# Kernel optimization log

Hardware: AMD Instinct MI355X
Metric: run time of the kernel (lower is better)

## Reference

```python
import jax, jax.numpy as jnp
import numpy as np

WS = 8          # window_size
NH = 8          # num_heads
IQKV = 128      # inner_qk_v_dim
IQKC = 32       # inner_qk_c_dim
IVV = 64        # inner_v_v_dim
EPS = 1e-6
B, HH, WW, DV, DC = 2, 224, 224, 256, 64


def _rmsnorm(x, g):
    return x * jax.lax.rsqrt(jnp.mean(x * x, axis=-1, keepdims=True) + EPS) * g


def _window(x):
    # (b, h, w, d) -> (b, Wh, Ww, ws*ws, d)
    b, h, w, d = x.shape
    x = x.reshape(b, h // WS, WS, w // WS, WS, d).transpose(0, 1, 3, 2, 4, 5)
    return x.reshape(b, h // WS, w // WS, WS * WS, d)


def _unwindow(x, h, w):
    # (b, N, ws*ws, d) -> (b, h, w, d)
    b, _, _, d = x.shape
    x = x.reshape(b, h // WS, w // WS, WS, WS, d).transpose(0, 1, 3, 2, 4, 5)
    return x.reshape(b, h, w, d)


def _source_qkv(V, C, Wqk_v, bqk_v, g_v, Wqk_c, bqk_c, g_c, Wv):
    Vw, Cw = _window(V), _window(C)          # (b, Wh, Ww, n, d)
    b, Wh, Ww, n, _ = Vw.shape
    N = Wh * Ww
    Vavg, Cavg = Vw.mean(-2), Cw.mean(-2)
    qk_v = _rmsnorm(Vavg @ Wqk_v + bqk_v, g_v)   # (b, Wh, Ww, 2*IQKV)
    qk_c = _rmsnorm(Cavg @ Wqk_c + bqk_c, g_c)   # (b, Wh, Ww, 2*IQKC)
    # 'b Wh Ww (H e) -> b H (Wh Ww) e' then chunk2 along e
    qk_v = qk_v.reshape(b, N, NH, -1).transpose(0, 2, 1, 3)
    qk_c = qk_c.reshape(b, N, NH, -1).transpose(0, 2, 1, 3)
    ev, ec = qk_v.shape[-1] // 2, qk_c.shape[-1] // 2
    qv, kv = qk_v[..., :ev], qk_v[..., ev:]
    qc, kc = qk_c[..., :ec], qk_c[..., ec:]
    # value projection: 'b Wh Ww n (e H) -> b H (Wh Ww) (n e)'
    e = IVV // NH
    Vv = (Vw @ Wv).reshape(b, N, n, e, NH).transpose(0, 4, 1, 2, 3).reshape(b, NH, N, n * e)
    return qv, kv, qc, kc, Vv, (Wh, Ww)


def _forward(values0, coords0, values1, coords1,
             Wqk_v, bqk_v, g_v, Wqk_c, bqk_c, g_c, Wv, Wback):
    parts = [_source_qkv(V, C, Wqk_v, bqk_v, g_v, Wqk_c, bqk_c, g_c, Wv)
             for V, C in ((values0, coords0), (values1, coords1))]
    qv = jnp.concatenate([p[0] for p in parts], axis=2)
    kv = jnp.concatenate([p[1] for p in parts], axis=2)
    qc = jnp.concatenate([p[2] for p in parts], axis=2)
    kc = jnp.concatenate([p[3] for p in parts], axis=2)
    Vv = jnp.concatenate([p[4] for p in parts], axis=2)
    scores = (jnp.einsum('bhqe,bhke->bhqk', qv, kv) / jnp.sqrt(jnp.float32(IQKV))
              + jnp.einsum('bhqe,bhke->bhqk', qc, kc) / jnp.sqrt(jnp.float32(IQKC)))
    A = jax.nn.softmax(scores, axis=-1)            # (b, H, N, N)
    rw = jnp.einsum('bhqk,bhkf->bhqf', A, Vv)      # (b, H, N, n*e)
    b, _, N, _ = rw.shape
    n, e = WS * WS, IVV // NH
    # 'b H N (n e) -> b N n (e H)'
    rw = rw.reshape(b, NH, N, n, e).transpose(0, 2, 3, 4, 1).reshape(b, N, n, e * NH)
    rw = rw @ Wback                                # (b, N, n, Dv)
    outs, off = [], 0
    for (V, _), p in zip(((values0, coords0), (values1, coords1)), parts):
        Wh, Ww = p[5]
        Ns = Wh * Ww
        outs.append(_unwindow(rw[:, off:off + Ns], Wh * WS, Ww * WS))
        off += Ns
    return tuple(outs)


def setup_inputs() -> dict:
    key = jax.random.key(0)
    ks = jax.random.split(key, 8)
    s = 0.02
    return {
        'values0': jax.random.normal(ks[0], (B, HH, WW, DV), jnp.float32),
        'coords0': jax.random.normal(ks[1], (B, HH, WW, DC), jnp.float32),
        'values1': jax.random.normal(ks[2], (B, HH, WW, DV), jnp.float32),
        'coords1': jax.random.normal(ks[3], (B, HH, WW, DC), jnp.float32),
        'Wqk_v': s * jax.random.normal(ks[4], (DV, 2 * IQKV), jnp.float32),
        'bqk_v': jnp.zeros((2 * IQKV,), jnp.float32),
        'g_v': jnp.ones((2 * IQKV,), jnp.float32),
        'Wqk_c': s * jax.random.normal(ks[5], (DC, 2 * IQKC), jnp.float32),
        'bqk_c': jnp.zeros((2 * IQKC,), jnp.float32),
        'g_c': jnp.ones((2 * IQKC,), jnp.float32),
        'Wv': s * jax.random.normal(ks[6], (DV, IVV), jnp.float32),
        'Wback': s * jax.random.normal(ks[7], (IVV, DV), jnp.float32),
    }


def reference(values0, coords0, values1, coords1,
              Wqk_v, bqk_v, g_v, Wqk_c, bqk_c, g_c, Wv, Wback):
    return _forward(values0, coords0, values1, coords1,
                    Wqk_v, bqk_v, g_v, Wqk_c, bqk_c, g_c, Wv, Wback)
```

## Files before the change

kernel.cpp:

```cpp
#include <hip/hip_runtime.h>

#define NSRC 784
#define NTOT 1568
#define NHD 8
#define DVC 256
#define DCC 64
#define D20 20
#define FDIM 512
#define OUT_PER_SRC 25690112

typedef short s16x8 __attribute__((ext_vector_type(8)));
typedef unsigned short u16x8 __attribute__((ext_vector_type(8)));
typedef unsigned short u16x4 __attribute__((ext_vector_type(4)));
typedef float f32x4 __attribute__((ext_vector_type(4)));
typedef float f32x16 __attribute__((ext_vector_type(16)));
typedef unsigned u32x4 __attribute__((ext_vector_type(4)));

__device__ __forceinline__ unsigned short f2bf(float x) {
    unsigned u = __float_as_uint(x);
    unsigned r = (u + 0x7FFFu + ((u >> 16) & 1u)) >> 16;
    return (unsigned short)r;
}

__device__ __forceinline__ unsigned cvt_pk_bf16(float lo, float hi) {
    unsigned r;
    asm volatile("v_cvt_pk_bf16_f32 %0, %1, %2" : "=v"(r) : "v"(lo), "v"(hi));
    return r;
}

__device__ __forceinline__ void split_bf(float x, unsigned short& hi, unsigned short& lo) {
    unsigned short h = f2bf(x);
    float hf = __uint_as_float(((unsigned)h) << 16);
    hi = h;
    lo = f2bf(x - hf);
}

__global__ __launch_bounds__(256) void kz_zero(unsigned short* __restrict__ p) {
    size_t i = (size_t)blockIdx.x * 256 + threadIdx.x;
    u16x8 z = (u16x8)0;
    *(u16x8*)&p[i * 8] = z;
}

__global__ __launch_bounds__(256) void k0_wsplit(
    const float* __restrict__ Wv,
    unsigned short* __restrict__ WThi, unsigned short* __restrict__ WTlo) {
    int e = blockIdx.x, dd = threadIdx.x;
    float x = Wv[dd * DCC + e];
    unsigned short h, l;
    split_bf(x, h, l);
    WThi[e * 256 + dd] = h;
    WTlo[e * 256 + dd] = l;
}

__global__ __launch_bounds__(256) void k0b_wback(
    const float* __restrict__ Wb, unsigned short* __restrict__ Wp) {
    int idx = blockIdx.x * 256 + threadIdx.x;
    int jj = idx & 7, lane = (idx >> 3) & 63, hl = (idx >> 9) & 1;
    int kc = (idx >> 10) & 1, mt = idx >> 11;
    int c = mt * 16 + (lane & 15);
    int j = kc * 32 + (lane >> 4) * 8 + jj;
    unsigned short h, l;
    split_bf(Wb[j * 256 + c], h, l);
    Wp[idx] = hl ? l : h;
}

__global__ __launch_bounds__(256) void k1c_avg(
    const float* __restrict__ c0, const float* __restrict__ c1,
    float* __restrict__ Cavg) {
    int wi = blockIdx.x * 4 + (threadIdx.x >> 6);
    int d = threadIdx.x & 63;
    int b = wi / NTOT, N = wi % NTOT;
    int src = N / NSRC, nloc = N % NSRC;
    int wh = nloc / 28, ww = nloc % 28;
    const float* __restrict__ C = src ? c1 : c0;
    int pbase = (b * 224 + wh * 8) * 224 + ww * 8;
    float s = 0.f;
#pragma unroll 8
    for (int p = 0; p < 64; ++p)
        s += C[(size_t)(pbase + (p >> 3) * 224 + (p & 7)) * DCC + d];
    Cavg[(size_t)wi * DCC + d] = s * 0.015625f;
}

__global__ __launch_bounds__(256) void k2_qk(
    const float* __restrict__ Vavg, const float* __restrict__ Cavg,
    const float* __restrict__ Wqkv, const float* __restrict__ bqkv, const float* __restrict__ gv,
    const float* __restrict__ Wqkc, const float* __restrict__ bqkc, const float* __restrict__ gc,
    unsigned short* __restrict__ Qp, unsigned short* __restrict__ Kp) {
    __shared__ float xv[DVC];
    __shared__ float xc[DCC];
    __shared__ float wred[4];
    int blk = blockIdx.x;
    int b = blk / NTOT, N = blk % NTOT;
    int t = threadIdx.x;
    int tile = N >> 5, l31 = N & 31;
    xv[t] = Vavg[(size_t)blk * DVC + t];
    if (t < DCC) xc[t] = Cavg[(size_t)blk * DCC + t];
    __syncthreads();
    float yv = bqkv[t];
#pragma unroll 4
    for (int d = 0; d < DVC; ++d) yv += xv[d] * Wqkv[d * 256 + t];
    float ss = yv * yv;
#pragma unroll
    for (int off = 32; off; off >>= 1) ss += __shfl_xor(ss, off, 64);
    if ((t & 63) == 0) wred[t >> 6] = ss;
    __syncthreads();
    float tot = wred[0] + wred[1] + wred[2] + wred[3];
    float rv = rsqrtf(tot * (1.f / 256.f) + 1e-6f);
    float yn = yv * rv * gv[t];
    int h = t >> 5, c = t & 31;
    int bh = b * NHD + h;
    {
        int isq = (c < 16);
        int d = isq ? c : c - 16;
        float val = isq ? yn * 0.088388347648318447f : yn;
        unsigned short h16, l16;
        split_bf(val, h16, l16);
        int hh = d >> 3, j = d & 7;
        size_t base = ((size_t)(bh * 49 + tile) * 4) * 512 + (size_t)(hh * 32 + l31) * 8 + j;
        unsigned short* dst = isq ? Qp : Kp;
        dst[base] = h16;
        dst[base + 1024] = l16;
    }
    if (t < DCC) {
        float yc = bqkc[t];
#pragma unroll 4
        for (int d = 0; d < DCC; ++d) yc += xc[d] * Wqkc[d * 64 + t];
        float sc = yc * yc;
#pragma unroll
        for (int off = 32; off; off >>= 1) sc += __shfl_xor(sc, off, 64);
        float rc = rsqrtf(sc * (1.f / 64.f) + 1e-6f);
        float ycn = yc * rc * gc[t];
        int h2 = t >> 3, c2 = t & 7;
        int bh2 = b * NHD + h2;
        int isq = (c2 < 4);
        int dd = isq ? c2 : c2 - 4;
        float val = isq ? ycn * 0.17677669529663687f : ycn;
        unsigned short h16, l16;
        split_bf(val, h16, l16);
        size_t base = ((size_t)(bh2 * 49 + tile) * 4 + 1) * 512 + (size_t)l31 * 8 + dd;
        unsigned short* dst = isq ? Qp : Kp;
        dst[base] = h16;
        dst[base + 1024] = l16;
    }
}

__global__ __launch_bounds__(256) void k3_vv(
    const float* __restrict__ v0, const float* __restrict__ v1,
    const unsigned short* __restrict__ WThi, const unsigned short* __restrict__ WTlo,
    unsigned short* __restrict__ Vvb, float* __restrict__ Vavg) {
    __shared__ unsigned short Ahi[64 * 128];
    __shared__ unsigned short Alo[64 * 128];
    int blk = blockIdx.x;
    int b = blk / NTOT, N = blk % NTOT;
    int src = N / NSRC, nloc = N % NSRC;
    int wh = nloc / 28, ww = nloc % 28;
    const float* __restrict__ V = src ? v1 : v0;
    int t = threadIdx.x;
    int w = t >> 6, lane = t & 63;
    int lm = lane & 15, lk = lane >> 4;
    int pxw = w * 16;
    int lhalf = lane >> 5;
    int d4 = (lane & 31) * 4;
    int pbase = (b * 224 + wh * 8) * 224 + ww * 8;

    float ap[8] = {0.f, 0.f, 0.f, 0.f, 0.f, 0.f, 0.f, 0.f};
    f32x4 acc4[4];
#pragma unroll
    for (int nt = 0; nt < 4; ++nt) acc4[nt] = (f32x4)0.f;

#pragma unroll
    for (int ph = 0; ph < 2; ++ph) {
        int d0 = ph * 128;
        float4 xs[8];
#pragma unroll
        for (int i = 0; i < 8; ++i) {
            int px = pxw + i * 2 + lhalf;
            xs[i] = *(const float4*)&V[(size_t)(pbase + (px >> 3) * 224 + (px & 7)) * DVC + d0 + d4];
        }
#pragma unroll
        for (int i = 0; i < 8; ++i) {
            ap[ph * 4 + 0] += xs[i].x; ap[ph * 4 + 1] += xs[i].y;
            ap[ph * 4 + 2] += xs[i].z; ap[ph * 4 + 3] += xs[i].w;
        }
        if (ph) __syncthreads();
#pragma unroll
        for (int i = 0; i < 8; ++i) {
            int px = pxw + i * 2 + lhalf;
            u16x4 h4, l4;
            unsigned short hq, lq;
            split_bf(xs[i].x, hq, lq); h4[0] = hq; l4[0] = lq;
            split_bf(xs[i].y, hq, lq); h4[1] = hq; l4[1] = lq;
            split_bf(xs[i].z, hq, lq); h4[2] = hq; l4[2] = lq;
            split_bf(xs[i].w, hq, lq); h4[3] = hq; l4[3] = lq;
            int addr = px * 128 + (((d4 >> 3) ^ (px & 7)) << 3) + (d4 & 7);
            *(u16x4*)&Ahi[addr] = h4;
            *(u16x4*)&Alo[addr] = l4;
        }
        __syncthreads();
#pragma unroll
        for (int c2 = 0; c2 < 4; ++c2) {
            int dd0 = c2 * 32;
            s16x8 Bh4[4], Bl4[4];
#pragma unroll
            for (int nt = 0; nt < 4; ++nt) {
                int e = nt * 16 + lm;
                Bh4[nt] = *(const s16x8*)&WThi[e * 256 + d0 + dd0 + lk * 8];
                Bl4[nt] = *(const s16x8*)&WTlo[e * 256 + d0 + dd0 + lk * 8];
            }
            int row = pxw + lm;
            int raddr = row * 128 + ((((dd0 >> 3) + lk) ^ (row & 7)) << 3);
            s16x8 ahi = *(const s16x8*)&Ahi[raddr];
            s16x8 alo = *(const s16x8*)&Alo[raddr];
#pragma unroll
            for (int nt = 0; nt < 4; ++nt) {
                acc4[nt] = __builtin_amdgcn_mfma_f32_16x16x32_bf16(ahi, Bl4[nt], acc4[nt], 0, 0, 0);
                acc4[nt] = __builtin_amdgcn_mfma_f32_16x16x32_bf16(alo, Bh4[nt], acc4[nt], 0, 0, 0);
                acc4[nt] = __builtin_amdgcn_mfma_f32_16x16x32_bf16(ahi, Bh4[nt], acc4[nt], 0, 0, 0);
            }
        }
    }
    __syncthreads();
    unsigned short* eb = Ahi;
#pragma unroll
    for (int nt = 0; nt < 4; ++nt) {
        int e = nt * 16 + lm;
#pragma unroll
        for (int r = 0; r < 4; ++r) {
            int px = pxw + lk * 4 + r;
            eb[px * 66 + e] = f2bf(acc4[nt][r]);
        }
    }
#pragma unroll
    for (int j = 0; j < 8; ++j) ap[j] += __shfl_xor(ap[j], 32, 64);
    float* avgb = (float*)Alo;
    if (lhalf == 0) {
#pragma unroll
        for (int ph = 0; ph < 2; ++ph) {
            float4 v4 = make_float4(ap[ph * 4], ap[ph * 4 + 1], ap[ph * 4 + 2], ap[ph * 4 + 3]);
            *(float4*)&avgb[w * 256 + ph * 128 + d4] = v4;
        }
    }
    __syncthreads();
    unsigned short* dst = Vvb + (size_t)blk * 4096;
#pragma unroll
    for (int i = 0; i < 2; ++i) {
        int flat16 = i * 256 + t;
        int f3 = flat16 >> 6;
        int h = (flat16 >> 3) & 7;
        int px8 = (flat16 & 7) * 8;
        u16x8 vv;
#pragma unroll
        for (int u = 0; u < 8; ++u) vv[u] = eb[(px8 + u) * 66 + f3 * 8 + h];
        *(u16x8*)&dst[flat16 * 8] = vv;
    }
    Vavg[(size_t)blk * DVC + t] =
        (avgb[t] + avgb[256 + t] + avgb[512 + t] + avgb[768 + t]) * 0.015625f;
}

__global__ __launch_bounds__(256) void k3b_pack(
    const unsigned short* __restrict__ Vvb, unsigned short* __restrict__ Vp) {
    __shared__ unsigned short tile[32 * 576];
    int kt = blockIdx.x, bh = blockIdx.y;
    int b = bh >> 3, h = bh & 7;
    int t = threadIdx.x;
#pragma unroll
    for (int it = 0; it < 8; ++it) {
        int flat = it * 256 + t;
        int r5 = flat >> 6;
        int c = flat & 63;
        int f3 = c >> 3, px8 = (c & 7) * 8;
        const unsigned short* s =
            Vvb + ((size_t)(b * NTOT + kt * 32 + r5) * 8 + f3) * 512 + h * 64 + px8;
        *(u16x8*)&tile[r5 * 576 + f3 * 72 + px8] = *(const u16x8*)s;
    }
    __syncthreads();
    unsigned short* dst = Vp + ((size_t)bh * 49 + kt) * 16384;
#pragma unroll
    for (int it = 0; it < 8; ++it) {
        int flato = it * 256 + t;
        int lane = flato & 63;
        int kh = (flato >> 6) & 1;
        int sub = (flato >> 7) & 3;
        int w = flato >> 9;
        int l31 = lane & 31, hh = lane >> 5;
        int f = w * 128 + sub * 32 + l31;
        int kbase = kh * 16 + hh * 8;
        u16x8 v;
#pragma unroll
        for (int j = 0; j < 8; ++j)
            v[j] = tile[(kbase + j) * 576 + (f & 7) * 72 + (f >> 3)];
        *(u16x8*)&dst[(size_t)flato * 8] = v;
    }
}

__global__ __launch_bounds__(256) void k4_attn(
    const unsigned short* __restrict__ Qp, const unsigned short* __restrict__ Kp,
    const unsigned short* __restrict__ Vp, float* __restrict__ rw) {
    __shared__ float ebuf[32 * 132];
    int wg = blockIdx.x;
    int qt = wg >> 4, bh = wg & 15;
    int q0 = qt * 32;
    int t = threadIdx.x;
    int w = t >> 6, lane = t & 63;
    int l31 = lane & 31, hh = lane >> 5;

    const unsigned short* __restrict__ Qpb = Qp + ((size_t)(bh * 49 + qt) * 4) * 512 + lane * 8;
    const unsigned short* __restrict__ Kpb = Kp + (size_t)bh * 49 * 2048 + lane * 8;
    const unsigned short* __restrict__ Vpb = Vp + (size_t)bh * 49 * 16384 + lane * 8;

    s16x8 qa0 = *(const s16x8*)&Qpb[0];
    s16x8 qa1 = *(const s16x8*)&Qpb[512];
    s16x8 ql0 = *(const s16x8*)&Qpb[1024];
    s16x8 ql1 = *(const s16x8*)&Qpb[1536];

    s16x8 ka0 = *(const s16x8*)&Kpb[0];
    s16x8 ka1 = *(const s16x8*)&Kpb[512];
    s16x8 kl0 = *(const s16x8*)&Kpb[1024];
    s16x8 kl1 = *(const s16x8*)&Kpb[1536];

    float m = -1e30f, lsum = 0.f;
    f32x16 acc[4];
#pragma unroll
    for (int s = 0; s < 4; ++s) acc[s] = (f32x16)0.f;

    for (int kt = 0; kt < NTOT / 32; ++kt) {
        const unsigned short* Vtile = Vpb + (size_t)kt * 16384 + (w * 8) * 512;
        s16x8 va[8];
#pragma unroll
        for (int fr = 0; fr < 8; ++fr)
            va[fr] = *(const s16x8*)&Vtile[fr * 512];
        int ktn = (kt < 48) ? kt + 1 : 48;
        const unsigned short* Ktn = Kpb + (size_t)ktn * 2048;
        s16x8 kn0 = *(const s16x8*)&Ktn[0];
        s16x8 kn1 = *(const s16x8*)&Ktn[512];
        s16x8 kn2 = *(const s16x8*)&Ktn[1024];
        s16x8 kn3 = *(const s16x8*)&Ktn[1536];

        f32x16 sacc = (f32x16)0.f;
        sacc = __builtin_amdgcn_mfma_f32_32x32x16_bf16(kl0, qa0, sacc, 0, 0, 0);
        sacc = __builtin_amdgcn_mfma_f32_32x32x16_bf16(ka0, ql0, sacc, 0, 0, 0);
        sacc = __builtin_amdgcn_mfma_f32_32x32x16_bf16(ka0, qa0, sacc, 0, 0, 0);
        sacc = __builtin_amdgcn_mfma_f32_32x32x16_bf16(kl1, qa1, sacc, 0, 0, 0);
        sacc = __builtin_amdgcn_mfma_f32_32x32x16_bf16(ka1, ql1, sacc, 0, 0, 0);
        sacc = __builtin_amdgcn_mfma_f32_32x32x16_bf16(ka1, qa1, sacc, 0, 0, 0);

        float tmax = sacc[0];
#pragma unroll
        for (int r = 1; r < 16; ++r) tmax = fmaxf(tmax, sacc[r]);
        tmax = fmaxf(tmax, __shfl_xor(tmax, 32, 64));
        if (__any(tmax > m + 8.f)) {
            float mn = fmaxf(m, tmax);
            float sc = __expf(m - mn);
#pragma unroll
            for (int s = 0; s < 4; ++s) acc[s] = acc[s] * sc;
            lsum *= sc;
            m = mn;
        }
        unsigned P2[8];
        float tsum = 0.f;
#pragma unroll
        for (int j = 0; j < 8; ++j) {
            float pa = __expf(sacc[2 * j] - m);
            float pb = __expf(sacc[2 * j + 1] - m);
            tsum += pa + pb;
            P2[j] = cvt_pk_bf16(pa, pb);
        }
        lsum += tsum + __shfl_xor(tsum, 32, 64);
        unsigned X2[8];
#pragma unroll
        for (int j = 0; j < 8; ++j) X2[j] = (unsigned)__shfl_xor((int)P2[j], 32, 64);
        u32x4 b0u, b1u;
        if (hh == 0) {
            b0u[0] = P2[0]; b0u[1] = P2[1]; b0u[2] = X2[0]; b0u[3] = X2[1];
            b1u[0] = P2[4]; b1u[1] = P2[5]; b1u[2] = X2[4]; b1u[3] = X2[5];
        } else {
            b0u[0] = X2[2]; b0u[1] = X2[3]; b0u[2] = P2[2]; b0u[3] = P2[3];
            b1u[0] = X2[6]; b1u[1] = X2[7]; b1u[2] = P2[6]; b1u[3] = P2[7];
        }
        s16x8 pb0 = __builtin_bit_cast(s16x8, b0u);
        s16x8 pb1 = __builtin_bit_cast(s16x8, b1u);

#pragma unroll
        for (int sub = 0; sub < 4; ++sub) {
            acc[sub] = __builtin_amdgcn_mfma_f32_32x32x16_bf16(va[2 * sub],     pb0, acc[sub], 0, 0, 0);
            acc[sub] = __builtin_amdgcn_mfma_f32_32x32x16_bf16(va[2 * sub + 1], pb1, acc[sub], 0, 0, 0);
        }
        ka0 = kn0; ka1 = kn1; kl0 = kn2; kl1 = kn3;
    }

    float inv = 1.f / lsum;
    float* rwg = rw + ((size_t)bh * NTOT + q0) * FDIM;
#pragma unroll
    for (int c = 0; c < 4; ++c) {
        __syncthreads();
        if (w == c) {
#pragma unroll
            for (int sub = 0; sub < 4; ++sub) {
#pragma unroll
                for (int r = 0; r < 16; ++r) {
                    int fl = sub * 32 + (r & 3) + 8 * (r >> 2) + 4 * hh;
                    ebuf[l31 * 132 + fl] = acc[sub][r] * inv;
                }
            }
        }
        __syncthreads();
        int qr = t >> 3, cb = (t & 7) * 16;
#pragma unroll
        for (int j = 0; j < 4; ++j) {
            *(float4*)&rwg[(size_t)qr * FDIM + c * 128 + cb + j * 4] =
                *(const float4*)&ebuf[qr * 132 + cb + j * 4];
        }
    }
}

__global__ __launch_bounds__(256) void k5_back(
    const float* __restrict__ rw, const unsigned short* __restrict__ Wp,
    float* __restrict__ out) {
    __shared__ unsigned short SB[2 * 64 * 72];
    unsigned short* BhL = SB;
    unsigned short* BlL = SB + 64 * 72;
    int blk = blockIdx.x;
    int b = blk / NTOT, N = blk % NTOT;
    int src = N / NSRC, nloc = N % NSRC;
    int wh = nloc / 28, ww = nloc % 28;
    int t = threadIdx.x;
    int w = t >> 6, lane = t & 63;
    int lm = lane & 15, lk = lane >> 4;
    int pbase = (b * 224 + wh * 8) * 224 + ww * 8;

#pragma unroll
    for (int i = 0; i < 4; ++i) {
        int flat4 = i * 256 + t;
        int h = flat4 >> 7;
        int f0 = (flat4 & 127) * 4;
        float4 v = *(const float4*)&rw[((size_t)(b * NHD + h) * NTOT + N) * FDIM + f0];
        int n = f0 >> 3;
        int ebase = f0 & 7;
        float vv[4] = {v.x, v.y, v.z, v.w};
#pragma unroll
        for (int u = 0; u < 4; ++u) {
            int j8 = ebase + u;
            unsigned short h16, l16;
            split_bf(vv[u], h16, l16);
            int col = ((j8 ^ (n & 7)) << 3) | h;
            BhL[n * 72 + col] = h16;
            BlL[n * 72 + col] = l16;
        }
    }
    __syncthreads();

    f32x4 acc[4][4];
#pragma unroll
    for (int mi = 0; mi < 4; ++mi)
#pragma unroll
        for (int nt = 0; nt < 4; ++nt) acc[mi][nt] = (f32x4)0.f;

    const unsigned short* Wpw = Wp + (size_t)(w * 4) * 2048 + lane * 8;
#pragma unroll
    for (int kc = 0; kc < 2; ++kc) {
        s16x8 Ah[4], Al[4], Bh4[4], Bl4[4];
#pragma unroll
        for (int mi = 0; mi < 4; ++mi) {
            int base = mi * 2048 + kc * 1024;
            Ah[mi] = *(const s16x8*)&Wpw[base];
            Al[mi] = *(const s16x8*)&Wpw[base + 512];
        }
#pragma unroll
        for (int nt = 0; nt < 4; ++nt) {
            int n = nt * 16 + lm;
            int addr = n * 72 + (((kc * 4 + lk) ^ (n & 7)) << 3);
            Bh4[nt] = *(const s16x8*)&BhL[addr];
            Bl4[nt] = *(const s16x8*)&BlL[addr];
        }
#pragma unroll
        for (int mi = 0; mi < 4; ++mi)
#pragma unroll
            for (int nt = 0; nt < 4; ++nt) {
                acc[mi][nt] = __builtin_amdgcn_mfma_f32_16x16x32_bf16(Ah[mi], Bl4[nt], acc[mi][nt], 0, 0, 0);
                acc[mi][nt] = __builtin_amdgcn_mfma_f32_16x16x32_bf16(Al[mi], Bh4[nt], acc[mi][nt], 0, 0, 0);
                acc[mi][nt] = __builtin_amdgcn_mfma_f32_16x16x32_bf16(Ah[mi], Bh4[nt], acc[mi][nt], 0, 0, 0);
            }
    }

    float* eb = (float*)SB;
    float* outp = out + (size_t)src * OUT_PER_SRC;
#pragma unroll
    for (int ch = 0; ch < 4; ++ch) {
        __syncthreads();
        if (w == ch) {
#pragma unroll
            for (int mi = 0; mi < 4; ++mi)
#pragma unroll
                for (int nt = 0; nt < 4; ++nt)
#pragma unroll
                    for (int r = 0; r < 4; ++r) {
                        int n = nt * 16 + lm;
                        int cl = mi * 16 + lk * 4 + r;
                        eb[n * 68 + cl] = acc[mi][nt][r];
                    }
        }
        __syncthreads();
#pragma unroll
        for (int i = 0; i < 4; ++i) {
            int fl4 = i * 256 + t;
            int n = fl4 >> 4, c4 = (fl4 & 15) * 4;
            int opix = pbase + (n >> 3) * 224 + (n & 7);
            *(float4*)&outp[(size_t)opix * DVC + ch * 64 + c4] =
                *(const float4*)&eb[n * 68 + c4];
        }
    }
}

extern "C" void kernel_launch(void* const* d_in, const int* in_sizes, int n_in,
                              void* d_out, int out_size, void* d_ws, size_t ws_size,
                              hipStream_t stream) {
    const float* v0   = (const float*)d_in[0];
    const float* c0   = (const float*)d_in[1];
    const float* v1   = (const float*)d_in[2];
    const float* c1   = (const float*)d_in[3];
    const float* Wqkv = (const float*)d_in[4];
    const float* bqkv = (const float*)d_in[5];
    const float* gv   = (const float*)d_in[6];
    const float* Wqkc = (const float*)d_in[7];
    const float* bqkc = (const float*)d_in[8];
    const float* gc   = (const float*)d_in[9];
    const float* Wv   = (const float*)d_in[10];
    const float* Wbk  = (const float*)d_in[11];

    float* ws = (float*)d_ws;
    float* rw   = ws;
    float* Vavg = ws;
    float* Cavg = ws + 802816;
    unsigned short* Qp   = (unsigned short*)(ws + 12845056);
    unsigned short* Kp   = (unsigned short*)(ws + 13647872);
    unsigned short* WThi = (unsigned short*)(ws + 14450688);
    unsigned short* WTlo = (unsigned short*)(ws + 14458880);
    unsigned short* Vvb  = (unsigned short*)(ws + 14467072);
    unsigned short* Vp   = (unsigned short*)(ws + 20889600);
    unsigned short* Wp   = (unsigned short*)(ws + 27312128);

    float* outp = (float*)d_out;

    kz_zero  <<<1568, 256, 0, stream>>>(Qp);
    k0_wsplit<<<64, 256, 0, stream>>>(Wv, WThi, WTlo);
    k0b_wback<<<256, 256, 0, stream>>>(Wbk, Wp);
    k3_vv    <<<2 * NTOT, 256, 0, stream>>>(v0, v1, WThi, WTlo, Vvb, Vavg);
    k1c_avg  <<<784, 256, 0, stream>>>(c0, c1, Cavg);
    k2_qk    <<<2 * NTOT, 256, 0, stream>>>(Vavg, Cavg, Wqkv, bqkv, gv, Wqkc, bqkc, gc, Qp, Kp);
    k3b_pack <<<dim3(49, 16), 256, 0, stream>>>(Vvb, Vp);
    k4_attn  <<<784, 256, 0, stream>>>(Qp, Kp, Vp, rw);
    k5_back  <<<2 * NTOT, 256, 0, stream>>>(rw, Wp, outp);
}
```

Baseline: 359.0 us.

## Feed window pixels directly as MFMA operands and prepack Wv in fragment layout

The value-projection kernel no longer stages split bf16 input tiles through shared memory. Each lane now loads its own pixel's eight channels straight from global memory and uses them as the B operand, with Wv prepacked hi/lo into MFMA fragment order so each weight fragment is one contiguous vector load. The per-window channel averages are computed with cross-lane shuffles instead of per-thread accumulation, which removes two barriers and the large LDS buffers. The cost is more shuffle work for the averages and strided 32-byte global loads per lane.

```diff
diff --git a/kernel.cpp b/kernel.cpp
--- a/kernel.cpp
+++ b/kernel.cpp
@@ -41,15 +41,16 @@
     *(u16x8*)&p[i * 8] = z;
 }
 
-__global__ __launch_bounds__(256) void k0_wsplit(
-    const float* __restrict__ Wv,
-    unsigned short* __restrict__ WThi, unsigned short* __restrict__ WTlo) {
-    int e = blockIdx.x, dd = threadIdx.x;
-    float x = Wv[dd * DCC + e];
+__global__ __launch_bounds__(256) void k0c_wvpack(
+    const float* __restrict__ Wv, unsigned short* __restrict__ Wvp) {
+    int idx = blockIdx.x * 256 + threadIdx.x;
+    int j = idx & 7, lane = (idx >> 3) & 63, hl = (idx >> 9) & 1;
+    int c = (idx >> 10) & 7, mi = idx >> 13;
+    int e = mi * 16 + (lane & 15);
+    int dd = c * 32 + (lane >> 4) * 8 + j;
     unsigned short h, l;
-    split_bf(x, h, l);
-    WThi[e * 256 + dd] = h;
-    WTlo[e * 256 + dd] = l;
+    split_bf(Wv[dd * DCC + e], h, l);
+    Wvp[idx] = hl ? l : h;
 }
 
 __global__ __launch_bounds__(256) void k0b_wback(
@@ -146,10 +147,10 @@
 
 __global__ __launch_bounds__(256) void k3_vv(
     const float* __restrict__ v0, const float* __restrict__ v1,
-    const unsigned short* __restrict__ WThi, const unsigned short* __restrict__ WTlo,
+    const unsigned short* __restrict__ Wvp,
     unsigned short* __restrict__ Vvb, float* __restrict__ Vavg) {
-    __shared__ unsigned short Ahi[64 * 128];
-    __shared__ unsigned short Alo[64 * 128];
+    __shared__ unsigned short eb[64 * 66];
+    __shared__ float avgw[1024];
     int blk = blockIdx.x;
     int b = blk / NTOT, N = blk % NTOT;
     int src = N / NSRC, nloc = N % NSRC;
@@ -158,86 +159,55 @@
     int t = threadIdx.x;
     int w = t >> 6, lane = t & 63;
     int lm = lane & 15, lk = lane >> 4;
-    int pxw = w * 16;
-    int lhalf = lane >> 5;
-    int d4 = (lane & 31) * 4;
+    int px = w * 16 + lm;
     int pbase = (b * 224 + wh * 8) * 224 + ww * 8;
-
-    float ap[8] = {0.f, 0.f, 0.f, 0.f, 0.f, 0.f, 0.f, 0.f};
-    f32x4 acc4[4];
-#pragma unroll
-    for (int nt = 0; nt < 4; ++nt) acc4[nt] = (f32x4)0.f;
-
-#pragma unroll
-    for (int ph = 0; ph < 2; ++ph) {
-        int d0 = ph * 128;
-        float4 xs[8];
-#pragma unroll
-        for (int i = 0; i < 8; ++i) {
-            int px = pxw + i * 2 + lhalf;
-            xs[i] = *(const float4*)&V[(size_t)(pbase + (px >> 3) * 224 + (px & 7)) * DVC + d0 + d4];
-        }
-#pragma unroll
-        for (int i = 0; i < 8; ++i) {
-            ap[ph * 4 + 0] += xs[i].x; ap[ph * 4 + 1] += xs[i].y;
-            ap[ph * 4 + 2] += xs[i].z; ap[ph * 4 + 3] += xs[i].w;
-        }
-        if (ph) __syncthreads();
-#pragma unroll
-        for (int i = 0; i < 8; ++i) {
-            int px = pxw + i * 2 + lhalf;
-            u16x4 h4, l4;
+    const float* __restrict__ xrow =
+        V + (size_t)(pbase + (px >> 3) * 224 + (px & 7)) * DVC + lk * 8;
+
+    f32x4 acc[4];
+#pragma unroll
+    for (int mi = 0; mi < 4; ++mi) acc[mi] = (f32x4)0.f;
+
+#pragma unroll
+    for (int c = 0; c < 8; ++c) {
+        float4 x0 = *(const float4*)&xrow[c * 32];
+        float4 x1 = *(const float4*)&xrow[c * 32 + 4];
+        float xv8[8] = {x0.x, x0.y, x0.z, x0.w, x1.x, x1.y, x1.z, x1.w};
+        u16x8 bhu, blu;
+#pragma unroll
+        for (int j = 0; j < 8; ++j) {
             unsigned short hq, lq;
-            split_bf(xs[i].x, hq, lq); h4[0] = hq; l4[0] = lq;
-            split_bf(xs[i].y, hq, lq); h4[1] = hq; l4[1] = lq;
-            split_bf(xs[i].z, hq, lq); h4[2] = hq; l4[2] = lq;
-            split_bf(xs[i].w, hq, lq); h4[3] = hq; l4[3] = lq;
-            int addr = px * 128 + (((d4 >> 3) ^ (px & 7)) << 3) + (d4 & 7);
-            *(u16x4*)&Ahi[addr] = h4;
-            *(u16x4*)&Alo[addr] = l4;
-        }
-        __syncthreads();
-#pragma unroll
-        for (int c2 = 0; c2 < 4; ++c2) {
-            int dd0 = c2 * 32;
-            s16x8 Bh4[4], Bl4[4];
-#pragma unroll
-            for (int nt = 0; nt < 4; ++nt) {
-                int e = nt * 16 + lm;
-                Bh4[nt] = *(const s16x8*)&WThi[e * 256 + d0 + dd0 + lk * 8];
-                Bl4[nt] = *(const s16x8*)&WTlo[e * 256 + d0 + dd0 + lk * 8];
-            }
-            int row = pxw + lm;
-            int raddr = row * 128 + ((((dd0 >> 3) + lk) ^ (row & 7)) << 3);
-            s16x8 ahi = *(const s16x8*)&Ahi[raddr];
-            s16x8 alo = *(const s16x8*)&Alo[raddr];
-#pragma unroll
-            for (int nt = 0; nt < 4; ++nt) {
-                acc4[nt] = __builtin_amdgcn_mfma_f32_16x16x32_bf16(ahi, Bl4[nt], acc4[nt], 0, 0, 0);
-                acc4[nt] = __builtin_amdgcn_mfma_f32_16x16x32_bf16(alo, Bh4[nt], acc4[nt], 0, 0, 0);
-                acc4[nt] = __builtin_amdgcn_mfma_f32_16x16x32_bf16(ahi, Bh4[nt], acc4[nt], 0, 0, 0);
-            }
-        }
-    }
-    __syncthreads();
-    unsigned short* eb = Ahi;
-#pragma unroll
-    for (int nt = 0; nt < 4; ++nt) {
-        int e = nt * 16 + lm;
+            split_bf(xv8[j], hq, lq);
+            bhu[j] = hq; blu[j] = lq;
+        }
+        s16x8 xhi = __builtin_bit_cast(s16x8, bhu);
+        s16x8 xlo = __builtin_bit_cast(s16x8, blu);
+        float sv[8] = {xv8[0], xv8[1], xv8[2], xv8[3], xv8[4], xv8[5], xv8[6], xv8[7]};
+#pragma unroll
+        for (int off = 1; off <= 8; off <<= 1)
+#pragma unroll
+            for (int j = 0; j < 8; ++j) sv[j] += __shfl_xor(sv[j], off, 64);
+        if (lm == 0) {
+#pragma unroll
+            for (int j = 0; j < 8; ++j)
+                avgw[w * 256 + c * 32 + lk * 8 + j] = sv[j];
+        }
+#pragma unroll
+        for (int mi = 0; mi < 4; ++mi) {
+            const unsigned short* Wf = Wvp + (size_t)((mi * 8 + c) * 2) * 512 + lane * 8;
+            s16x8 Ah = *(const s16x8*)&Wf[0];
+            s16x8 Al = *(const s16x8*)&Wf[512];
+            acc[mi] = __builtin_amdgcn_mfma_f32_16x16x32_bf16(Ah, xlo, acc[mi], 0, 0, 0);
+            acc[mi] = __builtin_amdgcn_mfma_f32_16x16x32_bf16(Al, xhi, acc[mi], 0, 0, 0);
+            acc[mi] = __builtin_amdgcn_mfma_f32_16x16x32_bf16(Ah, xhi, acc[mi], 0, 0, 0);
+        }
+    }
+#pragma unroll
+    for (int mi = 0; mi < 4; ++mi) {
 #pragma unroll
         for (int r = 0; r < 4; ++r) {
-            int px = pxw + lk * 4 + r;
-            eb[px * 66 + e] = f2bf(acc4[nt][r]);
-        }
-    }
-#pragma unroll
-    for (int j = 0; j < 8; ++j) ap[j] += __shfl_xor(ap[j], 32, 64);
-    float* avgb = (float*)Alo;
-    if (lhalf == 0) {
-#pragma unroll
-        for (int ph = 0; ph < 2; ++ph) {
-            float4 v4 = make_float4(ap[ph * 4], ap[ph * 4 + 1], ap[ph * 4 + 2], ap[ph * 4 + 3]);
-            *(float4*)&avgb[w * 256 + ph * 128 + d4] = v4;
+            int e = mi * 16 + lk * 4 + r;
+            eb[px * 66 + e] = f2bf(acc[mi][r]);
         }
     }
     __syncthreads();
@@ -254,7 +224,7 @@
         *(u16x8*)&dst[flat16 * 8] = vv;
     }
     Vavg[(size_t)blk * DVC + t] =
-        (avgb[t] + avgb[256 + t] + avgb[512 + t] + avgb[768 + t]) * 0.015625f;
+        (avgw[t] + avgw[256 + t] + avgw[512 + t] + avgw[768 + t]) * 0.015625f;
 }
 
 __global__ __launch_bounds__(256) void k3b_pack(
@@ -533,21 +503,20 @@
     float* Cavg = ws + 802816;
     unsigned short* Qp   = (unsigned short*)(ws + 12845056);
     unsigned short* Kp   = (unsigned short*)(ws + 13647872);
-    unsigned short* WThi = (unsigned short*)(ws + 14450688);
-    unsigned short* WTlo = (unsigned short*)(ws + 14458880);
+    unsigned short* Wvp  = (unsigned short*)(ws + 14450688);
     unsigned short* Vvb  = (unsigned short*)(ws + 14467072);
     unsigned short* Vp   = (unsigned short*)(ws + 20889600);
     unsigned short* Wp   = (unsigned short*)(ws + 27312128);
 
     float* outp = (float*)d_out;
 
-    kz_zero  <<<1568, 256, 0, stream>>>(Qp);
-    k0_wsplit<<<64, 256, 0, stream>>>(Wv, WThi, WTlo);
-    k0b_wback<<<256, 256, 0, stream>>>(Wbk, Wp);
-    k3_vv    <<<2 * NTOT, 256, 0, stream>>>(v0, v1, WThi, WTlo, Vvb, Vavg);
-    k1c_avg  <<<784, 256, 0, stream>>>(c0, c1, Cavg);
-    k2_qk    <<<2 * NTOT, 256, 0, stream>>>(Vavg, Cavg, Wqkv, bqkv, gv, Wqkc, bqkc, gc, Qp, Kp);
-    k3b_pack <<<dim3(49, 16), 256, 0, stream>>>(Vvb, Vp);
-    k4_attn  <<<784, 256, 0, stream>>>(Qp, Kp, Vp, rw);
-    k5_back  <<<2 * NTOT, 256, 0, stream>>>(rw, Wp, outp);
-}
+    kz_zero   <<<1568, 256, 0, stream>>>(Qp);
+    k0c_wvpack<<<256, 256, 0, stream>>>(Wv, Wvp);
+    k0b_wback <<<256, 256, 0, stream>>>(Wbk, Wp);
+    k3_vv     <<<2 * NTOT, 256, 0, stream>>>(v0, v1, Wvp, Vvb, Vavg);
+    k1c_avg   <<<784, 256, 0, stream>>>(c0, c1, Cavg);
+    k2_qk     <<<2 * NTOT, 256, 0, stream>>>(Vavg, Cavg, Wqkv, bqkv, gv, Wqkc, bqkc, gc, Qp, Kp);
+    k3b_pack  <<<dim3(49, 16), 256, 0, stream>>>(Vvb, Vp);
+    k4_attn   <<<784, 256, 0, stream>>>(Qp, Kp, Vp, rw);
+    k5_back   <<<2 * NTOT, 256, 0, stream>>>(rw, Wp, outp);
+}
```

Measured after the change: 335.6 us. 1.07x faster.
